# Kernel optimization log

Measured on AMD Instinct MI355X. Metric: run time of the kernel, lower is better.

Reference implementation:

```python
import jax, jax.numpy as jnp
import numpy as np

EPS = 1e-5
N_CAMERAS, N_POINTS = 6, 4


def _bilinear_sample(feats, gx, gy):
    # feats: [B, C, H, W]; gx, gy: [B, Q] in [-1, 1]; align_corners=False, zero padding
    B, C, H, W = feats.shape
    ix = ((gx + 1.0) * W - 1.0) * 0.5
    iy = ((gy + 1.0) * H - 1.0) * 0.5
    x0 = jnp.floor(ix)
    y0 = jnp.floor(iy)
    fx = ix - x0
    fy = iy - y0
    x0i = x0.astype(jnp.int32)
    y0i = y0.astype(jnp.int32)
    ff = feats.reshape(B, C, H * W)

    def corner(xi, yi, w):
        valid = (xi >= 0) & (xi < W) & (yi >= 0) & (yi < H)
        idx = jnp.clip(yi, 0, H - 1) * W + jnp.clip(xi, 0, W - 1)
        v = jnp.take_along_axis(ff, idx[:, None, :], axis=2)  # [B, C, Q]
        return v * (w * valid)[:, None, :]

    return (corner(x0i, y0i, (1 - fx) * (1 - fy))
            + corner(x0i + 1, y0i, fx * (1 - fy))
            + corner(x0i, y0i + 1, (1 - fx) * fy)
            + corner(x0i + 1, y0i + 1, fx * fy))


def setup_inputs() -> dict:
    key = jax.random.key(0)
    ks = jax.random.split(key, 8)
    Hb = Wb = 128
    nq = Hb * Wb
    bs, hidden, N, P = 2, 256, N_CAMERAS, N_POINTS
    C, Hf, Wf = 256, 28, 50

    rho = jnp.broadcast_to((jnp.arange(Hb, dtype=jnp.float32) / Hb)[:, None], (Hb, Wb))
    phi = jnp.broadcast_to((jnp.arange(Wb, dtype=jnp.float32) / Wb)[None, :], (Hb, Wb))
    pc_range = jnp.array([51.2, 2.0 * np.pi, -5.0, 3.0], jnp.float32)
    intervals = jnp.array([51.2 / Hb, 2.0 * np.pi / Wb], jnp.float32)
    img_size = jnp.array([1600.0, 900.0], jnp.float32)

    # realistic pinhole lidar->image matrices for 6 surround cameras
    K = np.array([[1200.0, 0, 800, 0], [0, 1200.0, 450, 0], [0, 0, 1, 0], [0, 0, 0, 1]], np.float32)
    mats = []
    for i in range(N):
        yaw = 2.0 * np.pi * i / N
        c, s = np.cos(yaw), np.sin(yaw)
        R = np.array([[s, -c, 0], [0, 0, -1], [c, s, 0]], np.float32)  # x_right, y_down, z_forward
        E = np.eye(4, dtype=np.float32)
        E[:3, :3] = R
        E[:3, 3] = np.array([0.0, 1.5, 0.5], np.float32)
        mats.append(K @ E)
    lidar2imgs = jnp.asarray(np.broadcast_to(np.stack(mats), (bs, N, 4, 4)).copy())

    return {
        'query': jax.random.normal(ks[0], (nq, bs, hidden), jnp.float32),
        'query_pos': jax.random.normal(ks[1], (nq, bs, hidden), jnp.float32),
        'rho': rho,
        'phi': phi,
        'zz_cord': jax.random.uniform(ks[2], (bs, nq, 1), jnp.float32),
        'img_feats': jax.random.normal(ks[3], (bs, N, C, Hf, Wf), jnp.float32),
        'lidar2imgs': lidar2imgs,
        'intervals': intervals,
        'pc_range': pc_range,
        'img_size': img_size,
        'Wa': jax.random.normal(ks[4], (hidden, N * P), jnp.float32) * 0.02,
        'ba': jnp.zeros((N * P,), jnp.float32),
        'Wo': jax.random.normal(ks[5], (hidden, hidden), jnp.float32) * 0.02,
        'bo': jnp.zeros((hidden,), jnp.float32),
    }


def reference(query, query_pos, rho, phi, zz_cord, img_feats, lidar2imgs,
              intervals, pc_range, img_size, Wa, ba, Wo, bo):
    q = jnp.transpose(query + query_pos, (1, 0, 2))  # [bs, nq, h]
    bs, nq, _ = q.shape
    aw = (q @ Wa + ba).reshape(bs, 1, nq, N_CAMERAS, N_POINTS)

    # polar BEV -> cartesian lidar coords
    r = rho.reshape(-1, 1) * pc_range[0] + intervals[0] / 2  # [nq, 1]
    p = phi.reshape(-1, 1) * pc_range[1] - jnp.pi + intervals[1] / 2
    xx = r * jnp.cos(p)
    yy = r * jnp.sin(p)
    zz = zz_cord * (pc_range[3] - pc_range[2]) + pc_range[2]  # [bs, nq, 1]
    xyz = jnp.concatenate([
        jnp.broadcast_to(xx[None], (bs, nq, 1)),
        jnp.broadcast_to(yy[None], (bs, nq, 1)),
        zz,
        jnp.ones((bs, nq, 1), q.dtype),
    ], axis=-1)  # [bs, nq, 4]

    cam = jnp.einsum('bnij,bqj->bnqi', lidar2imgs, xyz)  # [bs, N, nq, 4]
    zc = cam[..., 2]
    gx = cam[..., 0] / jnp.maximum(zc, EPS) / img_size[0]
    gy = cam[..., 1] / jnp.maximum(zc, EPS) / img_size[1]
    gx = (gx - 0.5) * 2.0
    gy = (gy - 0.5) * 2.0
    mask = (zc > EPS) & (gx > -1.0) & (gx < 1.0) & (gy > -1.0) & (gy < 1.0)  # [bs, N, nq]

    B, N, C, H, W = img_feats.shape
    sampled = _bilinear_sample(img_feats.reshape(B * N, C, H, W),
                               gx.reshape(B * N, nq), gy.reshape(B * N, nq))
    sampled = jnp.nan_to_num(sampled.reshape(B, N, C, nq).transpose(0, 2, 3, 1))  # [bs, C, nq, N]

    maskf = mask.transpose(0, 2, 1)[:, None, :, :, None].astype(q.dtype)  # [bs,1,nq,N,1]
    ws = (jax.nn.sigmoid(aw) * maskf).sum(-1)  # [bs, 1, nq, N]
    out = jnp.einsum('bcqn,bqn->bcq', sampled, ws[:, 0])  # [bs, C, nq]
    out = out.transpose(2, 0, 1) @ Wo + bo + query  # dropout p=0 -> identity
    mask_out = mask.transpose(0, 2, 1)[:, None, :, :, None]  # [bs,1,nq,N,1] bool
    return out, mask_out
```

## Files before the change

### kernel.cpp

```cpp
#include <hip/hip_runtime.h>
#include <math.h>

#define NQ    16384
#define BS    2
#define HID   256
#define NCAM  6
#define NPTS  4
#define CF    256
#define HF    28
#define WF    50
#define HWF   (HF*WF)
#define NIMG  (BS*NCAM)
#define EPSV  1e-5f

typedef __attribute__((ext_vector_type(8))) short short8v;
typedef __attribute__((ext_vector_type(4))) float float4v;

__device__ __forceinline__ unsigned short f2bf(float f) {
    unsigned u = __float_as_uint(f);
    u += 0x7fffu + ((u >> 16) & 1u);
    return (unsigned short)(u >> 16);
}
__device__ __forceinline__ float bfLO(unsigned u) { return __uint_as_float(u << 16); }
__device__ __forceinline__ float bfHI(unsigned u) { return __uint_as_float(u & 0xffff0000u); }

__global__ __launch_bounds__(256) void prep_aw(
    const float* __restrict__ feats, const float* __restrict__ Wo,
    const float* __restrict__ Wa,    const float* __restrict__ query,
    const float* __restrict__ query_pos, const float* __restrict__ ba,
    unsigned short* __restrict__ featsT, unsigned short* __restrict__ WoT,
    float* __restrict__ ws)
{
    __shared__ __align__(16) char smem[32 * 264 * 2];

    const int tx = threadIdx.x & 31;
    const int ty = threadIdx.x >> 5;
    if (blockIdx.x < 528) {
        float (*tile)[33] = reinterpret_cast<float(*)[33]>(smem);
        const int img = blockIdx.x / 44;
        const int hw0 = (blockIdx.x % 44) * 32;
        for (int ct = 0; ct < 8; ++ct) {
            const int c0 = ct * 32;
            #pragma unroll
            for (int i = 0; i < 4; ++i) {
                const int c  = c0 + ty + 8 * i;
                const int hw = hw0 + tx;
                tile[ty + 8 * i][tx] = (hw < HWF) ? feats[((size_t)img * CF + c) * HWF + hw] : 0.f;
            }
            __syncthreads();
            #pragma unroll
            for (int i = 0; i < 4; ++i) {
                const int hw = hw0 + ty + 8 * i;
                if (hw < HWF)
                    featsT[((size_t)img * HWF + hw) * CF + c0 + tx] = f2bf(tile[tx][ty + 8 * i]);
            }
            __syncthreads();
        }
    } else if (blockIdx.x < 592) {
        float (*tile)[33] = reinterpret_cast<float(*)[33]>(smem);
        const int bid = blockIdx.x - 528;
        const int kt = bid >> 3, nt = bid & 7;
        #pragma unroll
        for (int i = 0; i < 4; ++i)
            tile[ty + 8 * i][tx] = Wo[(size_t)(kt * 32 + ty + 8 * i) * HID + nt * 32 + tx];
        __syncthreads();
        #pragma unroll
        for (int i = 0; i < 4; ++i)
            WoT[(size_t)(nt * 32 + ty + 8 * i) * HID + kt * 32 + tx] = f2bf(tile[tx][ty + 8 * i]);
    } else {
        unsigned short (*waL)[264] = reinterpret_cast<unsigned short(*)[264]>(smem);
        #pragma unroll
        for (int s = 0; s < 32; ++s)
            waL[s][threadIdx.x] = (s < 24) ? f2bf(Wa[threadIdx.x * 24 + s]) : (unsigned short)0;
        __syncthreads();

        const int bid  = blockIdx.x - 592;
        const int wave = threadIdx.x >> 6;
        const int lane = threadIdx.x & 63;
        const int arow = lane & 15;
        const int g4   = lane >> 4;
        const int g0   = (bid * 4 + wave) * 16;
        const int ga   = g0 + arow;
        const int bb   = ga >> 14;
        const int qq   = ga & (NQ - 1);
        const float* qp1 = query     + ((size_t)qq * BS + bb) * HID;
        const float* qp2 = query_pos + ((size_t)qq * BS + bb) * HID;

        float4v aw0 = {0.f,0.f,0.f,0.f}, aw1 = {0.f,0.f,0.f,0.f};
        #pragma unroll
        for (int kk = 0; kk < 8; ++kk) {
            const int k0 = kk * 32 + g4 * 8;
            const float4 a0 = *reinterpret_cast<const float4*>(qp1 + k0);
            const float4 a1 = *reinterpret_cast<const float4*>(qp1 + k0 + 4);
            const float4 p0 = *reinterpret_cast<const float4*>(qp2 + k0);
            const float4 p1 = *reinterpret_cast<const float4*>(qp2 + k0 + 4);
            short8v af;
            af[0] = (short)f2bf(a0.x + p0.x); af[1] = (short)f2bf(a0.y + p0.y);
            af[2] = (short)f2bf(a0.z + p0.z); af[3] = (short)f2bf(a0.w + p0.w);
            af[4] = (short)f2bf(a1.x + p1.x); af[5] = (short)f2bf(a1.y + p1.y);
            af[6] = (short)f2bf(a1.z + p1.z); af[7] = (short)f2bf(a1.w + p1.w);
            const short8v b0 = *reinterpret_cast<const short8v*>(&waL[arow][k0]);
            const short8v b1 = *reinterpret_cast<const short8v*>(&waL[16 + arow][k0]);
            aw0 = __builtin_amdgcn_mfma_f32_16x16x32_bf16(af, b0, aw0, 0, 0, 0);
            aw1 = __builtin_amdgcn_mfma_f32_16x16x32_bf16(af, b1, aw1, 0, 0, 0);
        }
        const float ba0 = ba[arow];
        const float ba1 = (arow < 8) ? ba[16 + arow] : 0.f;
        #pragma unroll
        for (int i = 0; i < 4; ++i) {
            float s0 = 1.0f / (1.0f + __expf(-(aw0[i] + ba0)));
            float s1 = (arow < 8) ? 1.0f / (1.0f + __expf(-(aw1[i] + ba1))) : 0.f;
            s0 += __shfl_xor(s0, 1);  s0 += __shfl_xor(s0, 2);
            s1 += __shfl_xor(s1, 1);  s1 += __shfl_xor(s1, 2);
            if ((arow & 3) == 0) {
                const int gq = g0 + g4 * 4 + i;
                ws[(size_t)gq * 8 + (arow >> 2)] = s0;
                if (arow < 8)
                    ws[(size_t)gq * 8 + 4 + (arow >> 2)] = s1;
            }
        }
    }
}

__global__ __launch_bounds__(512) void ca_main8(
    const float* __restrict__ query, const float* __restrict__ rho,
    const float* __restrict__ phi,   const float* __restrict__ zz,
    const unsigned short* __restrict__ featsT, const float* __restrict__ l2i,
    const float* __restrict__ intervals, const float* __restrict__ pc_range,
    const float* __restrict__ img_size, const float* __restrict__ ws,
    const unsigned short* __restrict__ WoT, const float* __restrict__ bo,
    float* __restrict__ out)
{
    __shared__ char fab[16 * 512];

    const int tid  = threadIdx.x;
    const int wave = tid >> 6;
    const int lane = tid & 63;
    const int l32  = lane & 31;
    const int r    = wave * 2 + (lane >> 5);
    const int base = blockIdx.x * 16;
    const int g    = base + r;
    const int b    = g >> 14;
    const int q    = g & (NQ - 1);

    float gxs[NCAM], gys[NCAM];
    bool  msk[NCAM];
    {
        const float pc0 = pc_range[0], pc1 = pc_range[1];
        const float pc2 = pc_range[2], pc3 = pc_range[3];
        const float rr = rho[q] * pc0 + intervals[0] * 0.5f;
        const float pp = phi[q] * pc1 - 3.14159265358979323846f + intervals[1] * 0.5f;
        const float xx = rr * cosf(pp);
        const float yy = rr * sinf(pp);
        const float z  = zz[b * NQ + q] * (pc3 - pc2) + pc2;
        const float iw = img_size[0], ih = img_size[1];
        #pragma unroll
        for (int n = 0; n < NCAM; ++n) {
            const float* M = l2i + (b * NCAM + n) * 16;
            const float cx = M[0]*xx + M[1]*yy + M[2]*z  + M[3];
            const float cy = M[4]*xx + M[5]*yy + M[6]*z  + M[7];
            const float cz = M[8]*xx + M[9]*yy + M[10]*z + M[11];
            const float d  = fmaxf(cz, EPSV);
            const float gx = (cx / d / iw - 0.5f) * 2.0f;
            const float gy = (cy / d / ih - 0.5f) * 2.0f;
            msk[n] = (cz > EPSV) && (gx > -1.0f) && (gx < 1.0f)
                                 && (gy > -1.0f) && (gy < 1.0f);
            gxs[n] = gx; gys[n] = gy;
        }
    }
    if (l32 < NCAM)
        out[(size_t)NQ * BS * HID + ((size_t)b * NQ + q) * NCAM + l32] =
            msk[l32] ? 1.0f : 0.0f;

    float wsv[NCAM];
    {
        const float wsn = ws[(size_t)g * 8 + (l32 & 7)];
        #pragma unroll
        for (int n = 0; n < NCAM; ++n)
            wsv[n] = msk[n] ? __shfl(wsn, (lane & 32) + n) : 0.f;
    }

    float acc[8] = {0.f,0.f,0.f,0.f,0.f,0.f,0.f,0.f};
    for (int n = 0; n < NCAM; ++n) {
        if (msk[n]) {
            const float ixf = ((gxs[n] + 1.0f) * WF - 1.0f) * 0.5f;
            const float iyf = ((gys[n] + 1.0f) * HF - 1.0f) * 0.5f;
            const float x0f = floorf(ixf), y0f = floorf(iyf);
            const float fx = ixf - x0f, fy = iyf - y0f;
            const int x0 = (int)x0f, y0 = (int)y0f;
            const int   xs[4] = {x0, x0 + 1, x0,     x0 + 1};
            const int   ys[4] = {y0, y0,     y0 + 1, y0 + 1};
            const float wc[4] = {(1.f-fx)*(1.f-fy), fx*(1.f-fy),
                                 (1.f-fx)*fy,       fx*fy};
            const unsigned short* fb = featsT + (size_t)(b * NCAM + n) * HWF * CF + 8 * l32;
            #pragma unroll
            for (int c4 = 0; c4 < 4; ++c4) {
                const bool v = (xs[c4] >= 0) && (xs[c4] < WF) &&
                               (ys[c4] >= 0) && (ys[c4] < HF);
                const int xc = min(max(xs[c4], 0), WF - 1);
                const int yc = min(max(ys[c4], 0), HF - 1);
                const float wnv = wsv[n] * (v ? wc[c4] : 0.0f);
                const uint4 u = *reinterpret_cast<const uint4*>(fb + (size_t)(yc * WF + xc) * CF);
                acc[0] += wnv * bfLO(u.x); acc[1] += wnv * bfHI(u.x);
                acc[2] += wnv * bfLO(u.y); acc[3] += wnv * bfHI(u.y);
                acc[4] += wnv * bfLO(u.z); acc[5] += wnv * bfHI(u.z);
                acc[6] += wnv * bfLO(u.w); acc[7] += wnv * bfHI(u.w);
            }
        }
    }

    {
        uint4 u;
        u.x = ((unsigned)f2bf(acc[1]) << 16) | f2bf(acc[0]);
        u.y = ((unsigned)f2bf(acc[3]) << 16) | f2bf(acc[2]);
        u.z = ((unsigned)f2bf(acc[5]) << 16) | f2bf(acc[4]);
        u.w = ((unsigned)f2bf(acc[7]) << 16) | f2bf(acc[6]);
        *reinterpret_cast<uint4*>(fab + ((unsigned)(r * 512 + 16 * l32) ^ ((unsigned)(r & 7) << 4))) = u;
    }
    __syncthreads();

    const int colw = lane & 15;
    const int g4   = lane >> 4;
    #pragma unroll
    for (int t = 0; t < 2; ++t) {
        const int col = wave * 16 + t * 128 + colw;
        float4v dacc = {0.f,0.f,0.f,0.f};
        #pragma unroll
        for (int kk = 0; kk < 8; ++kk) {
            const int k0 = kk * 32 + g4 * 8;
            const short8v af = *reinterpret_cast<const short8v*>(
                fab + ((unsigned)(colw * 512 + k0 * 2) ^ ((unsigned)(colw & 7) << 4)));
            const short8v bw = *reinterpret_cast<const short8v*>(
                WoT + (size_t)col * HID + k0);
            dacc = __builtin_amdgcn_mfma_f32_16x16x32_bf16(af, bw, dacc, 0, 0, 0);
        }
        #pragma unroll
        for (int rg = 0; rg < 4; ++rg) {
            const int row = g4 * 4 + rg;
            const int gq = base + row;
            const int bq = gq >> 14, qq = gq & (NQ - 1);
            const size_t addr = ((size_t)qq * BS + bq) * HID + col;
            out[addr] = dacc[rg] + bo[col] + query[addr];
        }
    }
}

__global__ __launch_bounds__(256) void prep_all(
    const float* __restrict__ feats, const float* __restrict__ Wo,
    const float* __restrict__ Wa, unsigned short* __restrict__ featsT,
    unsigned short* __restrict__ WoT, unsigned short* __restrict__ WaT)
{
    __shared__ float tile[32][33];
    const int tx = threadIdx.x & 31;
    const int ty = threadIdx.x >> 5;
    if (blockIdx.x < 528) {
        const int img = blockIdx.x / 44;
        const int hw0 = (blockIdx.x % 44) * 32;
        for (int ct = 0; ct < 8; ++ct) {
            const int c0 = ct * 32;
            #pragma unroll
            for (int i = 0; i < 4; ++i) {
                const int c  = c0 + ty + 8 * i;
                const int hw = hw0 + tx;
                tile[ty + 8 * i][tx] = (hw < HWF) ? feats[((size_t)img * CF + c) * HWF + hw] : 0.f;
            }
            __syncthreads();
            #pragma unroll
            for (int i = 0; i < 4; ++i) {
                const int hw = hw0 + ty + 8 * i;
                if (hw < HWF)
                    featsT[((size_t)img * HWF + hw) * CF + c0 + tx] = f2bf(tile[tx][ty + 8 * i]);
            }
            __syncthreads();
        }
    } else if (blockIdx.x < 592) {
        const int bid = blockIdx.x - 528;
        const int kt = bid >> 3, nt = bid & 7;
        #pragma unroll
        for (int i = 0; i < 4; ++i)
            tile[ty + 8 * i][tx] = Wo[(size_t)(kt * 32 + ty + 8 * i) * HID + nt * 32 + tx];
        __syncthreads();
        #pragma unroll
        for (int i = 0; i < 4; ++i)
            WoT[(size_t)(nt * 32 + ty + 8 * i) * HID + kt * 32 + tx] = f2bf(tile[tx][ty + 8 * i]);
    } else {
        const int bid = blockIdx.x - 592;
        #pragma unroll
        for (int v = 0; v < 4; ++v) {
            const int idx = bid * 1024 + v * 256 + threadIdx.x;
            const int j = idx >> 8, k = idx & 255;
            WaT[idx] = (j < 24) ? f2bf(Wa[k * 24 + j]) : (unsigned short)0;
        }
    }
}

__global__ __launch_bounds__(512) void ca_fused3(
    const float* __restrict__ query, const float* __restrict__ query_pos,
    const float* __restrict__ rho,   const float* __restrict__ phi,
    const float* __restrict__ zz,    const unsigned short* __restrict__ featsT,
    const float* __restrict__ l2i,   const float* __restrict__ intervals,
    const float* __restrict__ pc_range, const float* __restrict__ img_size,
    const unsigned short* __restrict__ WaT, const float* __restrict__ ba,
    const unsigned short* __restrict__ WoT, const float* __restrict__ bo,
    float* __restrict__ out)
{
    __shared__ char  fab[16 * 512];
    __shared__ float awl[16][36];
    const int tid  = threadIdx.x;
    const int wave = tid >> 6;
    const int lane = tid & 63;
    const int l32  = lane & 31;
    const int r    = wave * 2 + (lane >> 5);
    const int base = blockIdx.x * 16;
    const int g    = base + r;
    const int b    = g >> 14;
    const int q    = g & (NQ - 1);
    const size_t qrow = ((size_t)q * BS + b) * HID;
    {
        const float4 a0 = *reinterpret_cast<const float4*>(&query[qrow + 8 * l32]);
        const float4 a1 = *reinterpret_cast<const float4*>(&query[qrow + 8 * l32 + 4]);
        const float4 p0 = *reinterpret_cast<const float4*>(&query_pos[qrow + 8 * l32]);
        const float4 p1 = *reinterpret_cast<const float4*>(&query_pos[qrow + 8 * l32 + 4]);
        uint4 u;
        u.x = ((unsigned)f2bf(a0.y + p0.y) << 16) | f2bf(a0.x + p0.x);
        u.y = ((unsigned)f2bf(a0.w + p0.w) << 16) | f2bf(a0.z + p0.z);
        u.z = ((unsigned)f2bf(a1.y + p1.y) << 16) | f2bf(a1.x + p1.x);
        u.w = ((unsigned)f2bf(a1.w + p1.w) << 16) | f2bf(a1.z + p1.z);
        *reinterpret_cast<uint4*>(fab + ((unsigned)(r * 512 + 16 * l32) ^ ((unsigned)(r & 7) << 4))) = u;
    }
    float gxs[NCAM], gys[NCAM];
    bool  msk[NCAM];
    {
        const float pc0 = pc_range[0], pc1 = pc_range[1];
        const float pc2 = pc_range[2], pc3 = pc_range[3];
        const float rr = rho[q] * pc0 + intervals[0] * 0.5f;
        const float pp = phi[q] * pc1 - 3.14159265358979323846f + intervals[1] * 0.5f;
        const float xx = rr * cosf(pp);
        const float yy = rr * sinf(pp);
        const float z  = zz[b * NQ + q] * (pc3 - pc2) + pc2;
        const float iw = img_size[0], ih = img_size[1];
        #pragma unroll
        for (int n = 0; n < NCAM; ++n) {
            const float* M = l2i + (b * NCAM + n) * 16;
            const float cx = M[0]*xx + M[1]*yy + M[2]*z  + M[3];
            const float cy = M[4]*xx + M[5]*yy + M[6]*z  + M[7];
            const float cz = M[8]*xx + M[9]*yy + M[10]*z + M[11];
            const float d  = fmaxf(cz, EPSV);
            const float gx = (cx / d / iw - 0.5f) * 2.0f;
            const float gy = (cy / d / ih - 0.5f) * 2.0f;
            msk[n] = (cz > EPSV) && (gx > -1.0f) && (gx < 1.0f)
                                 && (gy > -1.0f) && (gy < 1.0f);
            gxs[n] = gx; gys[n] = gy;
        }
    }
    if (l32 < NCAM)
        out[(size_t)NQ * BS * HID + ((size_t)b * NQ + q) * NCAM + l32] =
            msk[l32] ? 1.0f : 0.0f;
    __syncthreads();
    if (wave < 2) {
        const int arow = lane & 15;
        const int g4   = lane >> 4;
        float4v aw = {0.f,0.f,0.f,0.f};
        #pragma unroll
        for (int kk = 0; kk < 8; ++kk) {
            const int k0 = kk * 32 + g4 * 8;
            const short8v af = *reinterpret_cast<const short8v*>(
                fab + ((unsigned)(arow * 512 + k0 * 2) ^ ((unsigned)(arow & 7) << 4)));
            const short8v bw = *reinterpret_cast<const short8v*>(
                WaT + (size_t)(wave * 16 + arow) * HID + k0);
            aw = __builtin_amdgcn_mfma_f32_16x16x32_bf16(af, bw, aw, 0, 0, 0);
        }
        #pragma unroll
        for (int i = 0; i < 4; ++i)
            awl[g4 * 4 + i][wave * 16 + arow] = aw[i];
    }
    __syncthreads();
    float wsv[NCAM];
    {
        float sv = 0.f;
        if (l32 < 24) {
            const float x = awl[r][l32] + ba[l32];
            sv = 1.0f / (1.0f + __expf(-x));
        }
        sv += __shfl_xor(sv, 1);
        sv += __shfl_xor(sv, 2);
        #pragma unroll
        for (int n = 0; n < NCAM; ++n)
            wsv[n] = __shfl(sv, (lane & 32) + 4 * n);
    }
    float acc[8] = {0.f,0.f,0.f,0.f,0.f,0.f,0.f,0.f};
    for (int n = 0; n < NCAM; ++n) {
        if (msk[n]) {
            const float ixf = ((gxs[n] + 1.0f) * WF - 1.0f) * 0.5f;
            const float iyf = ((gys[n] + 1.0f) * HF - 1.0f) * 0.5f;
            const float x0f = floorf(ixf), y0f = floorf(iyf);
            const float fx = ixf - x0f, fy = iyf - y0f;
            const int x0 = (int)x0f, y0 = (int)y0f;
            const int   xs[4] = {x0, x0 + 1, x0,     x0 + 1};
            const int   ys[4] = {y0, y0,     y0 + 1, y0 + 1};
            const float wc[4] = {(1.f-fx)*(1.f-fy), fx*(1.f-fy),
                                 (1.f-fx)*fy,       fx*fy};
            const unsigned short* fb = featsT + (size_t)(b * NCAM + n) * HWF * CF + 8 * l32;
            #pragma unroll
            for (int c4 = 0; c4 < 4; ++c4) {
                const bool v = (xs[c4] >= 0) && (xs[c4] < WF) &&
                               (ys[c4] >= 0) && (ys[c4] < HF);
                const int xc = min(max(xs[c4], 0), WF - 1);
                const int yc = min(max(ys[c4], 0), HF - 1);
                const float wnv = wsv[n] * (v ? wc[c4] : 0.0f);
                const uint4 u = *reinterpret_cast<const uint4*>(fb + (size_t)(yc * WF + xc) * CF);
                acc[0] += wnv * bfLO(u.x); acc[1] += wnv * bfHI(u.x);
                acc[2] += wnv * bfLO(u.y); acc[3] += wnv * bfHI(u.y);
                acc[4] += wnv * bfLO(u.z); acc[5] += wnv * bfHI(u.z);
                acc[6] += wnv * bfLO(u.w); acc[7] += wnv * bfHI(u.w);
            }
        }
    }
    {
        uint4 u;
        u.x = ((unsigned)f2bf(acc[1]) << 16) | f2bf(acc[0]);
        u.y = ((unsigned)f2bf(acc[3]) << 16) | f2bf(acc[2]);
        u.z = ((unsigned)f2bf(acc[5]) << 16) | f2bf(acc[4]);
        u.w = ((unsigned)f2bf(acc[7]) << 16) | f2bf(acc[6]);
        *reinterpret_cast<uint4*>(fab + ((unsigned)(r * 512 + 16 * l32) ^ ((unsigned)(r & 7) << 4))) = u;
    }
    __syncthreads();
    const int colw = lane & 15;
    const int g4   = lane >> 4;
    #pragma unroll
    for (int t = 0; t < 2; ++t) {
        const int col = wave * 16 + t * 128 + colw;
        float4v dacc = {0.f,0.f,0.f,0.f};
        #pragma unroll
        for (int kk = 0; kk < 8; ++kk) {
            const int k0 = kk * 32 + g4 * 8;
            const short8v af = *reinterpret_cast<const short8v*>(
                fab + ((unsigned)(colw * 512 + k0 * 2) ^ ((unsigned)(colw & 7) << 4)));
            const short8v bw = *reinterpret_cast<const short8v*>(
                WoT + (size_t)col * HID + k0);
            dacc = __builtin_amdgcn_mfma_f32_16x16x32_bf16(af, bw, dacc, 0, 0, 0);
        }
        #pragma unroll
        for (int rg = 0; rg < 4; ++rg) {
            const int row = g4 * 4 + rg;
            const int gq = base + row;
            const int bq = gq >> 14, qq = gq & (NQ - 1);
            const size_t addr = ((size_t)qq * BS + bq) * HID + col;
            out[addr] = dacc[rg] + bo[col] + query[addr];
        }
    }
}

#define CHUNK 32
__global__ __launch_bounds__(512, 2) void ca_fused_fb(
    const float* __restrict__ query, const float* __restrict__ query_pos,
    const float* __restrict__ rho, const float* __restrict__ phi,
    const float* __restrict__ zz, const float* __restrict__ feats,
    const float* __restrict__ l2i, const float* __restrict__ intervals,
    const float* __restrict__ pc_range, const float* __restrict__ img_size,
    const float* __restrict__ Wa, const float* __restrict__ ba,
    const float* __restrict__ Wo, const float* __restrict__ bo,
    float* __restrict__ out)
{
    __shared__ float fa[8][HID];
    __shared__ float wolds[CHUNK][HID];
    const int tid  = threadIdx.x;
    const int wave = tid >> 6;
    const int lane = tid & 63;
    const int g    = blockIdx.x * 8 + wave;
    const int b    = g / NQ;
    const int q    = g - b * NQ;
    const size_t qrow = ((size_t)q * BS + b) * HID;
    {
        float qv[4];
        #pragma unroll
        for (int k = 0; k < 4; ++k) {
            const int h = lane + 64 * k;
            qv[k] = query[qrow + h] + query_pos[qrow + h];
        }
        const float pc0 = pc_range[0], pc1 = pc_range[1];
        const float pc2 = pc_range[2], pc3 = pc_range[3];
        const float r = rho[q] * pc0 + intervals[0] * 0.5f;
        const float p = phi[q] * pc1 - 3.14159265358979323846f + intervals[1] * 0.5f;
        const float xx = r * cosf(p);
        const float yy = r * sinf(p);
        const float z  = zz[b * NQ + q] * (pc3 - pc2) + pc2;
        const float iw = img_size[0], ih = img_size[1];
        float gxs[NCAM], gys[NCAM], wss[NCAM];
        bool  msk[NCAM];
        #pragma unroll
        for (int n = 0; n < NCAM; ++n) {
            const float* M = l2i + (b * NCAM + n) * 16;
            const float cx = M[0]*xx + M[1]*yy + M[2]*z  + M[3];
            const float cy = M[4]*xx + M[5]*yy + M[6]*z  + M[7];
            const float cz = M[8]*xx + M[9]*yy + M[10]*z + M[11];
            const float d  = fmaxf(cz, EPSV);
            const float gx = (cx / d / iw - 0.5f) * 2.0f;
            const float gy = (cy / d / ih - 0.5f) * 2.0f;
            msk[n] = (cz > EPSV) && (gx > -1.0f) && (gx < 1.0f)
                                 && (gy > -1.0f) && (gy < 1.0f);
            gxs[n] = gx; gys[n] = gy; wss[n] = 0.0f;
        }
        for (int n = 0; n < NCAM; ++n) {
            if (!msk[n]) continue;
            float s = 0.0f;
            #pragma unroll
            for (int pp = 0; pp < NPTS; ++pp) {
                const int j = n * NPTS + pp;
                float part = 0.0f;
                #pragma unroll
                for (int k = 0; k < 4; ++k)
                    part += qv[k] * Wa[(lane + 64 * k) * 24 + j];
                #pragma unroll
                for (int off = 32; off; off >>= 1)
                    part += __shfl_xor(part, off, 64);
                s += 1.0f / (1.0f + expf(-(part + ba[j])));
            }
            wss[n] = s;
        }
        if (lane < NCAM)
            out[(size_t)NQ * BS * HID + ((size_t)b * NQ + q) * NCAM + lane] =
                msk[lane] ? 1.0f : 0.0f;
        float acc[4] = {0.f,0.f,0.f,0.f};
        for (int n = 0; n < NCAM; ++n) {
            if (!msk[n]) continue;
            const float ixf = ((gxs[n] + 1.0f) * WF - 1.0f) * 0.5f;
            const float iyf = ((gys[n] + 1.0f) * HF - 1.0f) * 0.5f;
            const float x0f = floorf(ixf), y0f = floorf(iyf);
            const float fx = ixf - x0f, fy = iyf - y0f;
            const int x0 = (int)x0f, y0 = (int)y0f;
            const int   xs[4] = {x0, x0 + 1, x0,     x0 + 1};
            const int   ys[4] = {y0, y0,     y0 + 1, y0 + 1};
            const float wc[4] = {(1.f-fx)*(1.f-fy), fx*(1.f-fy),
                                 (1.f-fx)*fy,       fx*fy};
            int   offc[4];
            float wv[4];
            #pragma unroll
            for (int c4 = 0; c4 < 4; ++c4) {
                const bool v = (xs[c4] >= 0) && (xs[c4] < WF) &&
                               (ys[c4] >= 0) && (ys[c4] < HF);
                const int xc = min(max(xs[c4], 0), WF - 1);
                const int yc = min(max(ys[c4], 0), HF - 1);
                offc[c4] = yc * WF + xc;
                wv[c4]   = v ? wc[c4] : 0.0f;
            }
            const float wn = wss[n];
            const float* fbp = feats + (size_t)(b * NCAM + n) * CF * HWF;
            #pragma unroll
            for (int k = 0; k < 4; ++k) {
                const float* fc = fbp + (size_t)(lane + 64 * k) * HWF;
                const float sv = wv[0]*fc[offc[0]] + wv[1]*fc[offc[1]]
                               + wv[2]*fc[offc[2]] + wv[3]*fc[offc[3]];
                acc[k] += wn * sv;
            }
        }
        #pragma unroll
        for (int k = 0; k < 4; ++k)
            fa[wave][lane + 64 * k] = acc[k];
    }
    float racc[4] = {0.f,0.f,0.f,0.f};
    const int h0 = 4 * lane;
    for (int c0 = 0; c0 < HID; c0 += CHUNK) {
        __syncthreads();
        for (int i = tid; i < CHUNK * HID; i += 512)
            wolds[i >> 8][i & 255] = Wo[(size_t)(c0 + (i >> 8)) * HID + (i & 255)];
        __syncthreads();
        #pragma unroll 8
        for (int c = 0; c < CHUNK; ++c) {
            const float fav = fa[wave][c0 + c];
            const float4 wv4 = *reinterpret_cast<const float4*>(&wolds[c][h0]);
            racc[0] += fav * wv4.x;
            racc[1] += fav * wv4.y;
            racc[2] += fav * wv4.z;
            racc[3] += fav * wv4.w;
        }
    }
    float4 o;
    o.x = racc[0] + bo[h0 + 0] + query[qrow + h0 + 0];
    o.y = racc[1] + bo[h0 + 1] + query[qrow + h0 + 1];
    o.z = racc[2] + bo[h0 + 2] + query[qrow + h0 + 2];
    o.w = racc[3] + bo[h0 + 3] + query[qrow + h0 + 3];
    *reinterpret_cast<float4*>(&out[qrow + h0]) = o;
}

extern "C" void kernel_launch(void* const* d_in, const int* in_sizes, int n_in,
                              void* d_out, int out_size, void* d_ws, size_t ws_size,
                              hipStream_t stream) {
    const float* query     = (const float*)d_in[0];
    const float* query_pos = (const float*)d_in[1];
    const float* rho       = (const float*)d_in[2];
    const float* phi       = (const float*)d_in[3];
    const float* zz        = (const float*)d_in[4];
    const float* feats     = (const float*)d_in[5];
    const float* l2i       = (const float*)d_in[6];
    const float* intervals = (const float*)d_in[7];
    const float* pc_range  = (const float*)d_in[8];
    const float* img_size  = (const float*)d_in[9];
    const float* Wa        = (const float*)d_in[10];
    const float* ba        = (const float*)d_in[11];
    const float* Wo        = (const float*)d_in[12];
    const float* bo        = (const float*)d_in[13];
    float* out = (float*)d_out;

    const size_t featsT_bytes = (size_t)NIMG * HWF * CF * 2;
    const size_t woT_bytes    = (size_t)HID * HID * 2;
    const size_t waT_bytes    = (size_t)32 * HID * 2;
    const size_t ws_bytes     = (size_t)BS * NQ * 8 * 4;
    const size_t need_small   = featsT_bytes + woT_bytes + waT_bytes;
    const size_t need_full    = featsT_bytes + woT_bytes + ws_bytes;

    if (ws_size >= need_full) {
        unsigned short* featsT = (unsigned short*)d_ws;
        unsigned short* WoT    = (unsigned short*)((char*)d_ws + featsT_bytes);
        float*          wsb    = (float*)((char*)d_ws + featsT_bytes + woT_bytes);
        prep_aw<<<1104, 256, 0, stream>>>(feats, Wo, Wa, query, query_pos, ba,
                                          featsT, WoT, wsb);
        ca_main8<<<2048, 512, 0, stream>>>(query, rho, phi, zz, featsT, l2i,
                                           intervals, pc_range, img_size, wsb,
                                           WoT, bo, out);
    } else if (ws_size >= need_small) {
        unsigned short* featsT = (unsigned short*)d_ws;
        unsigned short* WoT    = (unsigned short*)((char*)d_ws + featsT_bytes);
        unsigned short* WaT    = (unsigned short*)((char*)d_ws + featsT_bytes + woT_bytes);
        prep_all<<<600, 256, 0, stream>>>(feats, Wo, Wa, featsT, WoT, WaT);
        ca_fused3<<<2048, 512, 0, stream>>>(query, query_pos, rho, phi, zz,
                                            featsT, l2i, intervals, pc_range,
                                            img_size, WaT, ba, WoT, bo, out);
    } else {
        ca_fused_fb<<<(BS * NQ) / 8, 512, 0, stream>>>(query, query_pos, rho, phi, zz,
                                                       feats, l2i, intervals, pc_range,
                                                       img_size, Wa, ba, Wo, bo, out);
    }
}
```

Baseline: 77.63 us.

## Split feature transpose across more blocks and make bilinear gathers branchless

The prep kernel now launches one block per 32x32 channel/pixel tile, 4224 blocks instead of 528 blocks that each looped over 8 channel tiles. This exposes more parallelism in the feature transpose. The main kernel computes all camera corner offsets and weights up front, with coordinates clamped to a safe range. It then issues all 24 gathers without the per-camera mask branch, so loads can be in flight together and wave divergence goes away. The cost is that masked cameras now fetch memory with zero weight, and register pressure goes up.

```diff
diff --git a/kernel.cpp b/kernel.cpp
--- a/kernel.cpp
+++ b/kernel.cpp
@@ -12,6 +12,7 @@
 #define HWF   (HF*WF)
 #define NIMG  (BS*NCAM)
 #define EPSV  1e-5f
+#define FB    4224
 
 typedef __attribute__((ext_vector_type(8))) short short8v;
 typedef __attribute__((ext_vector_type(4))) float float4v;
@@ -35,30 +36,28 @@
 
     const int tx = threadIdx.x & 31;
     const int ty = threadIdx.x >> 5;
-    if (blockIdx.x < 528) {
+    if (blockIdx.x < FB) {
         float (*tile)[33] = reinterpret_cast<float(*)[33]>(smem);
-        const int img = blockIdx.x / 44;
-        const int hw0 = (blockIdx.x % 44) * 32;
-        for (int ct = 0; ct < 8; ++ct) {
-            const int c0 = ct * 32;
-            #pragma unroll
-            for (int i = 0; i < 4; ++i) {
-                const int c  = c0 + ty + 8 * i;
-                const int hw = hw0 + tx;
-                tile[ty + 8 * i][tx] = (hw < HWF) ? feats[((size_t)img * CF + c) * HWF + hw] : 0.f;
-            }
-            __syncthreads();
-            #pragma unroll
-            for (int i = 0; i < 4; ++i) {
-                const int hw = hw0 + ty + 8 * i;
-                if (hw < HWF)
-                    featsT[((size_t)img * HWF + hw) * CF + c0 + tx] = f2bf(tile[tx][ty + 8 * i]);
-            }
-            __syncthreads();
-        }
-    } else if (blockIdx.x < 592) {
+        const int img = blockIdx.x / 352;
+        const int rem = blockIdx.x % 352;
+        const int hw0 = (rem % 44) * 32;
+        const int c0  = (rem / 44) * 32;
+        #pragma unroll
+        for (int i = 0; i < 4; ++i) {
+            const int c  = c0 + ty + 8 * i;
+            const int hw = hw0 + tx;
+            tile[ty + 8 * i][tx] = (hw < HWF) ? feats[((size_t)img * CF + c) * HWF + hw] : 0.f;
+        }
+        __syncthreads();
+        #pragma unroll
+        for (int i = 0; i < 4; ++i) {
+            const int hw = hw0 + ty + 8 * i;
+            if (hw < HWF)
+                featsT[((size_t)img * HWF + hw) * CF + c0 + tx] = f2bf(tile[tx][ty + 8 * i]);
+        }
+    } else if (blockIdx.x < FB + 64) {
         float (*tile)[33] = reinterpret_cast<float(*)[33]>(smem);
-        const int bid = blockIdx.x - 528;
+        const int bid = blockIdx.x - FB;
         const int kt = bid >> 3, nt = bid & 7;
         #pragma unroll
         for (int i = 0; i < 4; ++i)
@@ -74,7 +73,7 @@
             waL[s][threadIdx.x] = (s < 24) ? f2bf(Wa[threadIdx.x * 24 + s]) : (unsigned short)0;
         __syncthreads();
 
-        const int bid  = blockIdx.x - 592;
+        const int bid  = blockIdx.x - (FB + 64);
         const int wave = threadIdx.x >> 6;
         const int lane = threadIdx.x & 63;
         const int arow = lane & 15;
@@ -122,7 +121,7 @@
     }
 }
 
-__global__ __launch_bounds__(512) void ca_main8(
+__global__ __launch_bounds__(512) void ca_main9(
     const float* __restrict__ query, const float* __restrict__ rho,
     const float* __restrict__ phi,   const float* __restrict__ zz,
     const unsigned short* __restrict__ featsT, const float* __restrict__ l2i,
@@ -139,9 +138,11 @@
     const int l32  = lane & 31;
     const int r    = wave * 2 + (lane >> 5);
     const int base = blockIdx.x * 16;
+    const int b    = base >> 14;
     const int g    = base + r;
-    const int b    = g >> 14;
     const int q    = g & (NQ - 1);
+
+    const float wsn = ws[(size_t)g * 8 + (l32 & 7)];
 
     float gxs[NCAM], gys[NCAM];
     bool  msk[NCAM];
@@ -173,39 +174,48 @@
             msk[l32] ? 1.0f : 0.0f;
 
     float wsv[NCAM];
-    {
-        const float wsn = ws[(size_t)g * 8 + (l32 & 7)];
-        #pragma unroll
-        for (int n = 0; n < NCAM; ++n)
-            wsv[n] = msk[n] ? __shfl(wsn, (lane & 32) + n) : 0.f;
-    }
-
+    #pragma unroll
+    for (int n = 0; n < NCAM; ++n)
+        wsv[n] = msk[n] ? __shfl(wsn, (lane & 32) + n) : 0.f;
+
+    float wgt[NCAM][4];
+    int   off[NCAM][4];
+    #pragma unroll
+    for (int n = 0; n < NCAM; ++n) {
+        float ixf = ((gxs[n] + 1.0f) * WF - 1.0f) * 0.5f;
+        float iyf = ((gys[n] + 1.0f) * HF - 1.0f) * 0.5f;
+        ixf = fminf(fmaxf(ixf, -8.0f), 56.0f);
+        iyf = fminf(fmaxf(iyf, -8.0f), 34.0f);
+        const float x0f = floorf(ixf), y0f = floorf(iyf);
+        const float fx = ixf - x0f, fy = iyf - y0f;
+        const int x0 = (int)x0f, y0 = (int)y0f;
+        const int   xs[4] = {x0, x0 + 1, x0,     x0 + 1};
+        const int   ys[4] = {y0, y0,     y0 + 1, y0 + 1};
+        const float wc[4] = {(1.f-fx)*(1.f-fy), fx*(1.f-fy),
+                             (1.f-fx)*fy,       fx*fy};
+        #pragma unroll
+        for (int c4 = 0; c4 < 4; ++c4) {
+            const bool v = (xs[c4] >= 0) && (xs[c4] < WF) &&
+                           (ys[c4] >= 0) && (ys[c4] < HF);
+            const int xc = min(max(xs[c4], 0), WF - 1);
+            const int yc = min(max(ys[c4], 0), HF - 1);
+            off[n][c4] = yc * WF + xc;
+            wgt[n][c4] = wsv[n] * (v ? wc[c4] : 0.0f);
+        }
+    }
+    const unsigned short* fb0 = featsT + (size_t)b * (NCAM * HWF * CF) + 8 * l32;
     float acc[8] = {0.f,0.f,0.f,0.f,0.f,0.f,0.f,0.f};
+    #pragma unroll
     for (int n = 0; n < NCAM; ++n) {
-        if (msk[n]) {
-            const float ixf = ((gxs[n] + 1.0f) * WF - 1.0f) * 0.5f;
-            const float iyf = ((gys[n] + 1.0f) * HF - 1.0f) * 0.5f;
-            const float x0f = floorf(ixf), y0f = floorf(iyf);
-            const float fx = ixf - x0f, fy = iyf - y0f;
-            const int x0 = (int)x0f, y0 = (int)y0f;
-            const int   xs[4] = {x0, x0 + 1, x0,     x0 + 1};
-            const int   ys[4] = {y0, y0,     y0 + 1, y0 + 1};
-            const float wc[4] = {(1.f-fx)*(1.f-fy), fx*(1.f-fy),
-                                 (1.f-fx)*fy,       fx*fy};
-            const unsigned short* fb = featsT + (size_t)(b * NCAM + n) * HWF * CF + 8 * l32;
-            #pragma unroll
-            for (int c4 = 0; c4 < 4; ++c4) {
-                const bool v = (xs[c4] >= 0) && (xs[c4] < WF) &&
-                               (ys[c4] >= 0) && (ys[c4] < HF);
-                const int xc = min(max(xs[c4], 0), WF - 1);
-                const int yc = min(max(ys[c4], 0), HF - 1);
-                const float wnv = wsv[n] * (v ? wc[c4] : 0.0f);
-                const uint4 u = *reinterpret_cast<const uint4*>(fb + (size_t)(yc * WF + xc) * CF);
-                acc[0] += wnv * bfLO(u.x); acc[1] += wnv * bfHI(u.x);
-                acc[2] += wnv * bfLO(u.y); acc[3] += wnv * bfHI(u.y);
-                acc[4] += wnv * bfLO(u.z); acc[5] += wnv * bfHI(u.z);
-                acc[6] += wnv * bfLO(u.w); acc[7] += wnv * bfHI(u.w);
-            }
+        const unsigned short* fb = fb0 + (size_t)n * (HWF * CF);
+        #pragma unroll
+        for (int c4 = 0; c4 < 4; ++c4) {
+            const uint4 u = *reinterpret_cast<const uint4*>(fb + (size_t)off[n][c4] * CF);
+            const float w = wgt[n][c4];
+            acc[0] += w * bfLO(u.x); acc[1] += w * bfHI(u.x);
+            acc[2] += w * bfLO(u.y); acc[3] += w * bfHI(u.y);
+            acc[4] += w * bfLO(u.z); acc[5] += w * bfHI(u.z);
+            acc[6] += w * bfLO(u.w); acc[7] += w * bfHI(u.w);
         }
     }
 
@@ -613,9 +623,9 @@
         unsigned short* featsT = (unsigned short*)d_ws;
         unsigned short* WoT    = (unsigned short*)((char*)d_ws + featsT_bytes);
         float*          wsb    = (float*)((char*)d_ws + featsT_bytes + woT_bytes);
-        prep_aw<<<1104, 256, 0, stream>>>(feats, Wo, Wa, query, query_pos, ba,
+        prep_aw<<<4800, 256, 0, stream>>>(feats, Wo, Wa, query, query_pos, ba,
                                           featsT, WoT, wsb);
-        ca_main8<<<2048, 512, 0, stream>>>(query, rho, phi, zz, featsT, l2i,
+        ca_main9<<<2048, 512, 0, stream>>>(query, rho, phi, zz, featsT, l2i,
                                            intervals, pc_range, img_size, wsb,
                                            WoT, bo, out);
     } else if (ws_size >= need_small) {
```

New measurement: 85.17 us. 1.1x slower.
